# Kernel optimization log

Measured on AMD Instinct MI355X. Metric: run time of the kernel, lower is better.

## Reference

```python
import jax, jax.numpy as jnp
import numpy as np

K = 3
BN_EPS = 1e-3


def setup_inputs() -> dict:
    key = jax.random.key(0)
    ks = jax.random.split(key, 13)
    B, N1, N2 = 8, 1024, 4096
    C1, C2, Cs = 256, 128, 64
    Ctot = C1 + C2 + Cs  # 448
    H = 256
    return {
        "points1": jax.random.normal(ks[0], (B, 3, N1), jnp.float32),
        "points2": jax.random.normal(ks[1], (B, 3, N2), jnp.float32),
        "features1": jax.random.normal(ks[2], (B, C1, N1), jnp.float32),
        "features2": jax.random.normal(ks[3], (B, C2, N2), jnp.float32),
        "skip_features": jax.random.normal(ks[4], (B, Cs, N2), jnp.float32),
        # 1x1 Conv2d weights are equivalent to dense matrices [out, in]
        "W1": jax.random.normal(ks[5], (H, Ctot), jnp.float32) * 0.05,
        "b1": jax.random.normal(ks[6], (H,), jnp.float32) * 0.05,
        "g1": 1.0 + jax.random.normal(ks[7], (H,), jnp.float32) * 0.05,
        "beta1": jax.random.normal(ks[8], (H,), jnp.float32) * 0.05,
        "W2": jax.random.normal(ks[9], (H, H), jnp.float32) * 0.05,
        "b2": jax.random.normal(ks[10], (H,), jnp.float32) * 0.05,
        "g2": 1.0 + jax.random.normal(ks[11], (H,), jnp.float32) * 0.05,
        "beta2": jax.random.normal(ks[12], (H,), jnp.float32) * 0.05,
    }


def _conv_bn_relu(x, W, b, g, beta):
    # x: [B, N, Cin]; 1x1 conv == dense matmul per point
    y = jnp.einsum("bnc,oc->bno", x, W) + b
    # BatchNorm2d in training mode: batch stats over (batch, spatial) per channel
    mu = jnp.mean(y, axis=(0, 1))
    var = jnp.mean(jnp.square(y - mu), axis=(0, 1))  # biased variance
    y = (y - mu) * jax.lax.rsqrt(var + BN_EPS) * g + beta
    return jax.nn.relu(y)


def reference(points1, points2, features1, features2, skip_features,
              W1, b1, g1, beta1, W2, b2, g2, beta2):
    p1 = jnp.swapaxes(points1, 1, 2)  # [B, N1, 3]
    p2 = jnp.swapaxes(points2, 1, 2)  # [B, N2, 3]
    # pairwise Euclidean distances [B, N2, N1]
    d2 = (jnp.sum(p2 * p2, -1, keepdims=True)
          + jnp.sum(p1 * p1, -1)[:, None, :]
          - 2.0 * jnp.einsum("bnd,bmd->bnm", p2, p1))
    dist = jnp.sqrt(jnp.maximum(d2, 0.0))
    # k smallest distances
    neg_top, ind = jax.lax.top_k(-dist, K)  # ind: [B, N2, K]
    dk = -neg_top
    inv = 1.0 / (dk + 1e-10)
    w = inv / jnp.sum(inv, -1, keepdims=True)  # [B, N2, K]
    f1 = jnp.swapaxes(features1, 1, 2)  # [B, N1, C1]
    gathered = jax.vmap(lambda f, i: f[i])(f1, ind)  # [B, N2, K, C1]
    new = jnp.einsum("bnkc,bnk->bnc", gathered, w)  # inverse-distance interp
    x = jnp.concatenate([new,
                         jnp.swapaxes(features2, 1, 2),
                         jnp.swapaxes(skip_features, 1, 2)], axis=-1)
    x = _conv_bn_relu(x, W1, b1, g1, beta1)
    x = _conv_bn_relu(x, W2, b2, g2, beta2)
    return jnp.swapaxes(x, 1, 2)  # [B, Cout, N2]
```

## Files before the change

### kernel.cpp

```cpp
#include <hip/hip_runtime.h>
#include <cstdint>
#include <cstddef>

#define B_    8
#define N1_   1024
#define N2_   4096
#define C1_   256
#define C2_   128
#define CS_   64
#define CT_   448
#define H_    256
#define ROWS_ (B_ * N2_)

typedef __attribute__((ext_vector_type(8))) short bf16x8;
typedef __attribute__((ext_vector_type(4))) float f32x4;
typedef unsigned short ushort_t;
typedef unsigned int   uint_t;

__device__ __forceinline__ ushort_t f2bf(float f) {
    uint_t u = __float_as_uint(f);
    u = (u + 0x7fffu + ((u >> 16) & 1u)) >> 16;
    return (ushort_t)u;
}
__device__ __forceinline__ float bf2f(ushort_t h) {
    return __uint_as_float(((uint_t)h) << 16);
}
__device__ __forceinline__ void glds16(const void* g, void* l) {
    __builtin_amdgcn_global_load_lds(
        (const __attribute__((address_space(1))) void*)g,
        (__attribute__((address_space(3))) void*)l, 16, 0, 0);
}

__global__ __launch_bounds__(256) void fused_pre(
    const float* __restrict__ p1, const float* __restrict__ p2,
    int* __restrict__ ind, float* __restrict__ wout,
    const float* __restrict__ f1, const float* __restrict__ f2,
    const float* __restrict__ fs, const float* __restrict__ W1,
    const float* __restrict__ W2, ushort_t* __restrict__ f1t,
    ushort_t* __restrict__ x, ushort_t* __restrict__ W1b, ushort_t* __restrict__ W2b)
{
#pragma clang fp contract(off)
    __shared__ __align__(16) char smem[32000];
    const int t = threadIdx.x;
    const int bid = blockIdx.x;
    if (bid < 1024) {
        float4*   cand  = (float4*)(smem);
        float*    pvals = (float*)(smem + 16512);
        float*    thr   = (float*)(smem + 19584);
        ushort_t* lists = (ushort_t*)(smem + 19712);
        float*    pdd   = (float*)(smem + 25856);
        int*      pdi   = (int*)(smem + 28928);
        const int b  = bid >> 7;
        const int qb = (bid & 127) * 32;
        const float* pb1 = p1 + (size_t)b * 3 * N1_;
        for (int i = t; i < N1_; i += 256) {
            float X = pb1[i], Y = pb1[N1_ + i], Z = pb1[2 * N1_ + i];
            cand[i] = make_float4(X, Y, Z, (X * X + Y * Y) + Z * Z);
        }
        const int q = t & 31, split = t >> 5;
        const int n = qb + q;
        const float* pb2 = p2 + (size_t)b * 3 * N2_;
        const float ax = pb2[n], ay = pb2[N2_ + n], az = pb2[2 * N2_ + n];
        const float s2a = (ax * ax + ay * ay) + az * az;
        const float m2x = -2.0f * ax, m2y = -2.0f * ay, m2z = -2.0f * az;
        __syncthreads();
        const int ibeg = split * 128, iend = ibeg + 128;
        {
            float a0 = 3e38f, a1 = 3e38f, a2 = 3e38f;
            for (int i = ibeg; i < iend; ++i) {
                float4 c = cand[i];
                float fd = fmaf(c.x, m2x, fmaf(c.y, m2y, fmaf(c.z, m2z, s2a + c.w)));
                float o0 = a0, o1 = a1;
                a0 = fminf(o0, fd);
                a1 = __builtin_amdgcn_fmed3f(fd, o0, o1);
                a2 = __builtin_amdgcn_fmed3f(fd, o1, a2);
            }
            pvals[t * 3 + 0] = a0; pvals[t * 3 + 1] = a1; pvals[t * 3 + 2] = a2;
        }
        __syncthreads();
        if (t < 32) {
            float m0 = 3e38f, m1 = 3e38f, m2v = 3e38f;
#pragma unroll
            for (int g = 0; g < 8; ++g)
#pragma unroll
                for (int r = 0; r < 3; ++r) {
                    float v = pvals[(g * 32 + t) * 3 + r];
                    float o0 = m0, o1 = m1;
                    m0 = fminf(o0, v);
                    m1 = __builtin_amdgcn_fmed3f(v, o0, o1);
                    m2v = __builtin_amdgcn_fmed3f(v, o1, m2v);
                }
            thr[t] = m2v + 2e-3f;
        }
        __syncthreads();
        const float th = thr[q];
        ushort_t* mylist = lists + (q * 8 + split) * 12;
        int cnt = 0;
        for (int i = ibeg; i < iend; ++i) {
            float4 c = cand[i];
            float fd = fmaf(c.x, m2x, fmaf(c.y, m2y, fmaf(c.z, m2z, s2a + c.w)));
            if (fd <= th && cnt < 12) { mylist[cnt] = (ushort_t)i; cnt++; }
        }
        float e0 = 3e38f, e1 = 3e38f, e2 = 3e38f;
        int   j0 = 0, j1 = 0, j2 = 0;
        for (int k = 0; k < cnt; ++k) {
            const int i = mylist[k];
            float4 c = cand[i];
            float dot = (ax * c.x + ay * c.y) + az * c.z;
            float dd  = (s2a + c.w) - 2.0f * dot;
            float d   = sqrtf(fmaxf(dd, 0.0f));
            if (d < e0)      { e2 = e1; j2 = j1; e1 = e0; j1 = j0; e0 = d; j0 = i; }
            else if (d < e1) { e2 = e1; j2 = j1; e1 = d;  j1 = i; }
            else if (d < e2) { e2 = d;  j2 = i; }
        }
        pdd[(split * 32 + q) * 3 + 0] = e0; pdi[(split * 32 + q) * 3 + 0] = j0;
        pdd[(split * 32 + q) * 3 + 1] = e1; pdi[(split * 32 + q) * 3 + 1] = j1;
        pdd[(split * 32 + q) * 3 + 2] = e2; pdi[(split * 32 + q) * 3 + 2] = j2;
        __syncthreads();
        if (t < 32) {
            float f0 = 3e38f, f1v = 3e38f, f2v = 3e38f;
            int   k0 = 0, k1 = 0, k2 = 0;
#pragma unroll
            for (int g = 0; g < 8; ++g)
#pragma unroll
                for (int r = 0; r < 3; ++r) {
                    float d = pdd[(g * 32 + t) * 3 + r];
                    int   i = pdi[(g * 32 + t) * 3 + r];
                    if (d < f0)       { f2v = f1v; k2 = k1; f1v = f0; k1 = k0; f0 = d; k0 = i; }
                    else if (d < f1v) { f2v = f1v; k2 = k1; f1v = d;  k1 = i; }
                    else if (d < f2v) { f2v = d;  k2 = i; }
                }
            float inv0 = 1.0f / (f0 + 1e-10f);
            float inv1 = 1.0f / (f1v + 1e-10f);
            float inv2 = 1.0f / (f2v + 1e-10f);
            float s = (inv0 + inv1) + inv2;
            const size_t row = (size_t)b * N2_ + qb + t;
            wout[row * 3 + 0] = inv0 / s;
            wout[row * 3 + 1] = inv1 / s;
            wout[row * 3 + 2] = inv2 / s;
            ind[row * 3 + 0] = k0;
            ind[row * 3 + 1] = k1;
            ind[row * 3 + 2] = k2;
        }
    } else if (bid < 1536) {
        float (*tile)[65] = (float (*)[65])smem;
        const int bid2 = bid - 1024;
        const int b  = bid2 >> 6;
        const int ct = (bid2 >> 4) & 3;
        const int nt = bid2 & 15;
        const int c0 = ct * 64, n0 = nt * 64;
        const float* src = f1 + ((size_t)b * C1_ + c0) * N1_ + n0;
#pragma unroll
        for (int j = 0; j < 16; ++j) {
            int lin = j * 256 + t;
            int ci = lin >> 6, nj = lin & 63;
            tile[ci][nj] = src[(size_t)ci * N1_ + nj];
        }
        __syncthreads();
        ushort_t* dst = f1t + ((size_t)b * N1_ + n0) * C1_ + c0;
#pragma unroll
        for (int j = 0; j < 8; ++j) {
            int lin = j * 256 + t;
            int ni = lin >> 5, cjp = (lin & 31) * 2;
            uint_t u = (uint_t)f2bf(tile[cjp][ni]) | ((uint_t)f2bf(tile[cjp + 1][ni]) << 16);
            *(uint_t*)&dst[(size_t)ni * C1_ + cjp] = u;
        }
    } else if (bid < 3072) {
        float (*tile)[65] = (float (*)[65])smem;
        const int bid2 = bid - 1536;
        const int b   = bid2 / 192;
        const int rem = bid2 - b * 192;
        const int ct  = rem >> 6;
        const int nt  = rem & 63;
        const float* src;
        int coff;
        if (ct < 2) { src = f2 + ((size_t)b * C2_ + ct * 64) * N2_; coff = C1_ + ct * 64; }
        else        { src = fs + (size_t)b * CS_ * N2_;             coff = C1_ + C2_; }
        const int n0 = nt * 64;
#pragma unroll
        for (int j = 0; j < 16; ++j) {
            int lin = j * 256 + t;
            int ci = lin >> 6, nj = lin & 63;
            tile[ci][nj] = src[(size_t)ci * N2_ + n0 + nj];
        }
        __syncthreads();
#pragma unroll
        for (int j = 0; j < 8; ++j) {
            int lin = j * 256 + t;
            int ni = lin >> 5, cjp = (lin & 31) * 2;
            uint_t u = (uint_t)f2bf(tile[cjp][ni]) | ((uint_t)f2bf(tile[cjp + 1][ni]) << 16);
            *(uint_t*)&x[((size_t)b * N2_ + n0 + ni) * CT_ + coff + cjp] = u;
        }
    } else {
        const int i = (bid - 3072) * 256 + t;
        if (i < H_ * CT_) W1b[i] = f2bf(W1[i]);
        if (i < H_ * H_)  W2b[i] = f2bf(W2[i]);
    }
}

__global__ __launch_bounds__(256) void gather_x(
    const ushort_t* __restrict__ f1t, const int* __restrict__ ind,
    const float* __restrict__ w, ushort_t* __restrict__ x)
{
    const int t = threadIdx.x;
    const int row = blockIdx.x * 8 + (t >> 5);
    const int b = row >> 12;
    const int cg = (t & 31) * 8;
    const int*   ip = ind + (size_t)row * 3;
    const float* wp = w   + (size_t)row * 3;
    const int i0 = ip[0], i1 = ip[1], i2 = ip[2];
    const float w0 = wp[0], w1 = wp[1], w2 = wp[2];
    const ushort_t* base = f1t + (size_t)b * N1_ * C1_;
    uint4 va = *(const uint4*)(base + (size_t)i0 * C1_ + cg);
    uint4 vb = *(const uint4*)(base + (size_t)i1 * C1_ + cg);
    uint4 vc = *(const uint4*)(base + (size_t)i2 * C1_ + cg);
    const uint_t* pa = (const uint_t*)&va;
    const uint_t* pb = (const uint_t*)&vb;
    const uint_t* pc = (const uint_t*)&vc;
    uint_t out[4];
#pragma unroll
    for (int e = 0; e < 4; ++e) {
        float lo = w0 * bf2f((ushort_t)(pa[e] & 0xffff))
                 + w1 * bf2f((ushort_t)(pb[e] & 0xffff))
                 + w2 * bf2f((ushort_t)(pc[e] & 0xffff));
        float hi = w0 * bf2f((ushort_t)(pa[e] >> 16))
                 + w1 * bf2f((ushort_t)(pb[e] >> 16))
                 + w2 * bf2f((ushort_t)(pc[e] >> 16));
        out[e] = (uint_t)f2bf(lo) | ((uint_t)f2bf(hi) << 16);
    }
    *(uint4*)&x[(size_t)row * CT_ + cg] = *(uint4*)out;
}

__global__ __launch_bounds__(256, 4) void gemm1_glds(
    const ushort_t* __restrict__ A, const ushort_t* __restrict__ Bw,
    const float* __restrict__ bias, ushort_t* __restrict__ C,
    float* __restrict__ ssum, float* __restrict__ ssq)
{
    __shared__ __align__(16) ushort_t smem[12288];
    ushort_t* As = smem;
    ushort_t* Bs = smem + 8192;
    ushort_t* Cs = smem;
    const int t = threadIdx.x;
    const int m0 = (blockIdx.x >> 2) * 128;
    const int n0 = (blockIdx.x & 3) * 64;
    const int lane = t & 63;
    const int wv = t >> 6;
    const int wrow = wv & 1, wcol = wv >> 1;
    const int lm = lane & 15, lq = lane >> 4;
    const int lrow8  = lane >> 3;
    const int lchunk = (lane & 7) ^ lrow8;
    const ushort_t* gA = A  + (size_t)(m0 + wv * 32 + lrow8) * CT_ + lchunk * 8;
    const ushort_t* gB = Bw + (size_t)(n0 + wv * 16 + lrow8) * CT_ + lchunk * 8;
    ushort_t* lA = As + wv * 2048;
    ushort_t* lB = Bs + wv * 1024;
    const int aswz = lm & 7;
    f32x4 acc[4][2];
#pragma unroll
    for (int i = 0; i < 4; ++i)
#pragma unroll
        for (int j = 0; j < 2; ++j)
            acc[i][j] = (f32x4){0.f, 0.f, 0.f, 0.f};

    for (int k0 = 0; k0 < CT_; k0 += 64) {
        __syncthreads();
#pragma unroll
        for (int g = 0; g < 4; ++g)
            glds16(gA + k0 + g * 8 * CT_, lA + g * 512);
#pragma unroll
        for (int g = 0; g < 2; ++g)
            glds16(gB + k0 + g * 8 * CT_, lB + g * 512);
        __syncthreads();
#pragma unroll
        for (int h = 0; h < 2; ++h) {
            bf16x8 af[4], bfr[2];
#pragma unroll
            for (int i = 0; i < 4; ++i)
                af[i] = *(const bf16x8*)&As[(wrow * 64 + i * 16 + lm) * 64
                                            + (((h * 4 + lq) ^ aswz)) * 8];
#pragma unroll
            for (int j = 0; j < 2; ++j)
                bfr[j] = *(const bf16x8*)&Bs[(wcol * 32 + j * 16 + lm) * 64
                                             + (((h * 4 + lq) ^ aswz)) * 8];
#pragma unroll
            for (int i = 0; i < 4; ++i)
#pragma unroll
                for (int j = 0; j < 2; ++j)
                    acc[i][j] = __builtin_amdgcn_mfma_f32_16x16x32_bf16(af[i], bfr[j], acc[i][j], 0, 0, 0);
        }
    }
    __syncthreads();
#pragma unroll
    for (int j = 0; j < 2; ++j) {
        const int gn_l = wcol * 32 + j * 16 + lm;
        const int gn   = n0 + gn_l;
        const float bb = bias[gn];
        float ps = 0.0f, pq = 0.0f;
#pragma unroll
        for (int i = 0; i < 4; ++i) {
            const int row_l = wrow * 64 + i * 16 + lq * 4;
            f32x4 v = acc[i][j];
#pragma unroll
            for (int r = 0; r < 4; ++r) {
                float val = v[r] + bb;
                ps += val;
                pq += val * val;
                float vo = __shfl_xor(val, 1);
                uint_t packed = (lm & 1)
                    ? ((uint_t)f2bf(vo)  | ((uint_t)f2bf(val) << 16))
                    : ((uint_t)f2bf(val) | ((uint_t)f2bf(vo)  << 16));
                if ((lm & 1) == 0)
                    *(uint_t*)&Cs[(row_l + r) * 72 + (gn_l & ~1)] = packed;
            }
        }
        ps += __shfl_xor(ps, 16); pq += __shfl_xor(pq, 16);
        ps += __shfl_xor(ps, 32); pq += __shfl_xor(pq, 32);
        if (lane < 16) {
            atomicAdd(&ssum[gn], ps);
            atomicAdd(&ssq[gn], pq);
        }
    }
    __syncthreads();
    const int srow = t >> 3;
    const int scol = (t & 7) * 8;
#pragma unroll
    for (int rep = 0; rep < 4; ++rep) {
        const int row = srow + rep * 32;
        uint4 v = *(const uint4*)&Cs[row * 72 + scol];
        *(uint4*)(C + (size_t)(m0 + row) * H_ + n0 + scol) = v;
    }
}

__global__ __launch_bounds__(256, 4) void gemm2_fused(
    const ushort_t* __restrict__ A, const ushort_t* __restrict__ Bw,
    const float* __restrict__ bias,
    const float* __restrict__ s1, const float* __restrict__ q1,
    const float* __restrict__ g1, const float* __restrict__ be1,
    ushort_t* __restrict__ C, float* __restrict__ ssum, float* __restrict__ ssq)
{
    __shared__ __align__(16) ushort_t smem[15360];
    ushort_t* As0 = smem;
    ushort_t* As1 = smem + 5120;
    ushort_t* Bs  = smem + 10240;
    float*    sc  = (float*)(smem + 14336);
    float*    sh  = (float*)(smem + 14848);
    ushort_t* Cs  = smem;
    const int t = threadIdx.x;
    const int m0 = (blockIdx.x >> 2) * 128;
    const int n0 = (blockIdx.x & 3) * 64;
    const int lane = t & 63;
    const int wv = t >> 6;
    const int wrow = wv & 1, wcol = wv >> 1;
    const int lm = lane & 15, lq = lane >> 4;
    const int lrow8  = lane >> 3;
    const int lchunk = (lane & 7) ^ lrow8;
    const int aswz = lm & 7;
    const int arow = t >> 1, acol = (t & 1) * 32;
    {
        const float invN = 1.0f / (float)ROWS_;
        float mu  = s1[t] * invN;
        float var = q1[t] * invN - mu * mu;
        float s   = rsqrtf(var + 1e-3f) * g1[t];
        sc[t] = s;
        sh[t] = be1[t] - mu * s;
    }
    const ushort_t* gB = Bw + (size_t)(n0 + wv * 16 + lrow8) * H_ + lchunk * 8;
    ushort_t* lB = Bs + wv * 1024;
    const ushort_t* gA = A + (size_t)(m0 + arow) * H_ + acol;
    ushort_t* As_t = (t & 1) ? As1 : As0;
    f32x4 acc[4][2];
#pragma unroll
    for (int i = 0; i < 4; ++i)
#pragma unroll
        for (int j = 0; j < 2; ++j)
            acc[i][j] = (f32x4){0.f, 0.f, 0.f, 0.f};

    for (int k0 = 0; k0 < H_; k0 += 64) {
        uint4 av[4];
#pragma unroll
        for (int g = 0; g < 4; ++g)
            av[g] = *(const uint4*)(gA + k0 + g * 8);
        __syncthreads();
#pragma unroll
        for (int g = 0; g < 2; ++g)
            glds16(gB + k0 + g * 8 * H_, lB + g * 512);
#pragma unroll
        for (int g = 0; g < 4; ++g) {
            const uint_t* wsrc = (const uint_t*)&av[g];
            uint_t o[4];
#pragma unroll
            for (int e = 0; e < 4; ++e) {
                const int cb = k0 + acol + g * 8 + 2 * e;
                float lo = __uint_as_float(wsrc[e] << 16);
                float hi = __uint_as_float(wsrc[e] & 0xffff0000u);
                float r0 = fmaxf(fmaf(lo, sc[cb],     sh[cb]),     0.0f);
                float r1 = fmaxf(fmaf(hi, sc[cb + 1], sh[cb + 1]), 0.0f);
                o[e] = (uint_t)f2bf(r0) | ((uint_t)f2bf(r1) << 16);
            }
            *(uint4*)&As_t[arow * 40 + g * 8] = *(uint4*)o;
        }
        __syncthreads();
#pragma unroll
        for (int h = 0; h < 2; ++h) {
            const ushort_t* Ah = h ? As1 : As0;
            bf16x8 af[4], bfr[2];
#pragma unroll
            for (int i = 0; i < 4; ++i)
                af[i] = *(const bf16x8*)&Ah[(wrow * 64 + i * 16 + lm) * 40 + lq * 8];
#pragma unroll
            for (int j = 0; j < 2; ++j)
                bfr[j] = *(const bf16x8*)&Bs[(wcol * 32 + j * 16 + lm) * 64
                                             + (((h * 4 + lq) ^ aswz)) * 8];
#pragma unroll
            for (int i = 0; i < 4; ++i)
#pragma unroll
                for (int j = 0; j < 2; ++j)
                    acc[i][j] = __builtin_amdgcn_mfma_f32_16x16x32_bf16(af[i], bfr[j], acc[i][j], 0, 0, 0);
        }
    }
    __syncthreads();
#pragma unroll
    for (int j = 0; j < 2; ++j) {
        const int gn_l = wcol * 32 + j * 16 + lm;
        const int gn   = n0 + gn_l;
        const float bb = bias[gn];
        float ps = 0.0f, pq = 0.0f;
#pragma unroll
        for (int i = 0; i < 4; ++i) {
            const int row_l = wrow * 64 + i * 16 + lq * 4;
            f32x4 v = acc[i][j];
#pragma unroll
            for (int r = 0; r < 4; ++r) {
                float val = v[r] + bb;
                ps += val;
                pq += val * val;
                float vo = __shfl_xor(val, 1);
                uint_t packed = (lm & 1)
                    ? ((uint_t)f2bf(vo)  | ((uint_t)f2bf(val) << 16))
                    : ((uint_t)f2bf(val) | ((uint_t)f2bf(vo)  << 16));
                if ((lm & 1) == 0)
                    *(uint_t*)&Cs[(row_l + r) * 72 + (gn_l & ~1)] = packed;
            }
        }
        ps += __shfl_xor(ps, 16); pq += __shfl_xor(pq, 16);
        ps += __shfl_xor(ps, 32); pq += __shfl_xor(pq, 32);
        if (lane < 16) {
            atomicAdd(&ssum[gn], ps);
            atomicAdd(&ssq[gn], pq);
        }
    }
    __syncthreads();
    const int srow = t >> 3;
    const int scol = (t & 7) * 8;
#pragma unroll
    for (int rep = 0; rep < 4; ++rep) {
        const int row = srow + rep * 32;
        uint4 v = *(const uint4*)&Cs[row * 72 + scol];
        *(uint4*)(C + (size_t)(m0 + row) * H_ + n0 + scol) = v;
    }
}

__global__ __launch_bounds__(256) void bn_out_kernel(
    const ushort_t* __restrict__ y, const float* __restrict__ ssum, const float* __restrict__ ssq,
    const float* __restrict__ g, const float* __restrict__ beta, float* __restrict__ out)
{
    __shared__ float tile[64][65];
    __shared__ float sc[64], sh[64];
    const float invN = 1.0f / (float)ROWS_;
    const int bid = blockIdx.x;
    const int b  = bid >> 8;
    const int nt = (bid >> 2) & 63;
    const int ot = bid & 3;
    const int t = threadIdx.x;
    if (t < 64) {
        int c = ot * 64 + t;
        float mu  = ssum[c] * invN;
        float var = ssq[c] * invN - mu * mu;
        float s   = rsqrtf(var + 1e-3f) * g[c];
        sc[t] = s;
        sh[t] = beta[c] - mu * s;
    }
    __syncthreads();
    const int n0 = nt * 64, o0 = ot * 64;
    const ushort_t* yb = y + ((size_t)b * N2_ + n0) * H_ + o0;
#pragma unroll
    for (int j = 0; j < 8; ++j) {
        int lin = j * 256 + t;
        int nl = lin >> 5, cu = (lin & 31) * 2;
        uint_t u = *(const uint_t*)&yb[(size_t)nl * H_ + cu];
        tile[nl][cu]     = fmaxf(bf2f((ushort_t)(u & 0xffff)) * sc[cu]     + sh[cu],     0.0f);
        tile[nl][cu + 1] = fmaxf(bf2f((ushort_t)(u >> 16))    * sc[cu + 1] + sh[cu + 1], 0.0f);
    }
    __syncthreads();
    float* ob = out + ((size_t)b * H_ + o0) * N2_ + n0;
#pragma unroll
    for (int j = 0; j < 16; ++j) {
        int lin = j * 256 + t;
        int ol = lin >> 6, nl = lin & 63;
        ob[(size_t)ol * N2_ + nl] = tile[nl][ol];
    }
}

extern "C" void kernel_launch(void* const* d_in, const int* in_sizes, int n_in,
                              void* d_out, int out_size, void* d_ws, size_t ws_size,
                              hipStream_t stream)
{
    (void)in_sizes; (void)n_in; (void)out_size; (void)ws_size;
    const float* points1   = (const float*)d_in[0];
    const float* points2   = (const float*)d_in[1];
    const float* features1 = (const float*)d_in[2];
    const float* features2 = (const float*)d_in[3];
    const float* skipf     = (const float*)d_in[4];
    const float* W1  = (const float*)d_in[5];
    const float* b1  = (const float*)d_in[6];
    const float* g1  = (const float*)d_in[7];
    const float* be1 = (const float*)d_in[8];
    const float* W2  = (const float*)d_in[9];
    const float* b2  = (const float*)d_in[10];
    const float* g2  = (const float*)d_in[11];
    const float* be2 = (const float*)d_in[12];
    float* out = (float*)d_out;

    char* ws = (char*)d_ws;
    float*    s1  = (float*)(ws + 0);
    float*    q1  = (float*)(ws + 1024);
    float*    s2  = (float*)(ws + 2048);
    float*    q2  = (float*)(ws + 3072);
    int*      ind = (int*)(ws + 4096);
    float*    wgt = (float*)(ws + 397312);
    ushort_t* x   = (ushort_t*)(ws + 790528);
    ushort_t* y1b = (ushort_t*)(ws + 30150656);
    ushort_t* W1b = (ushort_t*)(ws + 63705088);
    ushort_t* W2b = (ushort_t*)(ws + 63934464);
    ushort_t* f1t = (ushort_t*)(ws + 64065536);
    ushort_t* y2b = x;

    hipMemsetAsync(ws, 0, 4096, stream);

    fused_pre<<<dim3(3520), dim3(256), 0, stream>>>(points1, points2, ind, wgt,
                                                    features1, features2, skipf,
                                                    W1, W2, f1t, x, W1b, W2b);
    gather_x<<<dim3(4096), dim3(256), 0, stream>>>(f1t, ind, wgt, x);

    gemm1_glds<<<dim3(ROWS_ / 128 * 4), dim3(256), 0, stream>>>(x, W1b, b1, y1b, s1, q1);
    gemm2_fused<<<dim3(ROWS_ / 128 * 4), dim3(256), 0, stream>>>(y1b, W2b, b2, s1, q1, g1, be1, y2b, s2, q2);
    bn_out_kernel<<<dim3(2048), dim3(256), 0, stream>>>(y2b, s2, q2, g2, be2, out);
}
```

Baseline: 199.0 us.

## Fuse inverse-distance gather into first GEMM A-tile loading

Result: faster. 190.6 us (-4.2%).

```diff
diff --git a/kernel.cpp b/kernel.cpp
--- a/kernel.cpp
+++ b/kernel.cpp
@@ -11,6 +11,7 @@
 #define CT_   448
 #define H_    256
 #define ROWS_ (B_ * N2_)
+#define XW_   192
 
 typedef __attribute__((ext_vector_type(8))) short bf16x8;
 typedef __attribute__((ext_vector_type(4))) float f32x4;
@@ -173,9 +174,9 @@
         const int ct  = rem >> 6;
         const int nt  = rem & 63;
         const float* src;
-        int coff;
-        if (ct < 2) { src = f2 + ((size_t)b * C2_ + ct * 64) * N2_; coff = C1_ + ct * 64; }
-        else        { src = fs + (size_t)b * CS_ * N2_;             coff = C1_ + C2_; }
+        if (ct < 2) src = f2 + ((size_t)b * C2_ + ct * 64) * N2_;
+        else        src = fs + (size_t)b * CS_ * N2_;
+        const int coff = ct * 64;
         const int n0 = nt * 64;
 #pragma unroll
         for (int j = 0; j < 16; ++j) {
@@ -189,7 +190,7 @@
             int lin = j * 256 + t;
             int ni = lin >> 5, cjp = (lin & 31) * 2;
             uint_t u = (uint_t)f2bf(tile[cjp][ni]) | ((uint_t)f2bf(tile[cjp + 1][ni]) << 16);
-            *(uint_t*)&x[((size_t)b * N2_ + n0 + ni) * CT_ + coff + cjp] = u;
+            *(uint_t*)&x[((size_t)b * N2_ + n0 + ni) * XW_ + coff + cjp] = u;
         }
     } else {
         const int i = (bid - 3072) * 256 + t;
@@ -198,43 +199,11 @@
     }
 }
 
-__global__ __launch_bounds__(256) void gather_x(
+__global__ __launch_bounds__(256, 4) void gemm1_fused(
     const ushort_t* __restrict__ f1t, const int* __restrict__ ind,
-    const float* __restrict__ w, ushort_t* __restrict__ x)
-{
-    const int t = threadIdx.x;
-    const int row = blockIdx.x * 8 + (t >> 5);
-    const int b = row >> 12;
-    const int cg = (t & 31) * 8;
-    const int*   ip = ind + (size_t)row * 3;
-    const float* wp = w   + (size_t)row * 3;
-    const int i0 = ip[0], i1 = ip[1], i2 = ip[2];
-    const float w0 = wp[0], w1 = wp[1], w2 = wp[2];
-    const ushort_t* base = f1t + (size_t)b * N1_ * C1_;
-    uint4 va = *(const uint4*)(base + (size_t)i0 * C1_ + cg);
-    uint4 vb = *(const uint4*)(base + (size_t)i1 * C1_ + cg);
-    uint4 vc = *(const uint4*)(base + (size_t)i2 * C1_ + cg);
-    const uint_t* pa = (const uint_t*)&va;
-    const uint_t* pb = (const uint_t*)&vb;
-    const uint_t* pc = (const uint_t*)&vc;
-    uint_t out[4];
-#pragma unroll
-    for (int e = 0; e < 4; ++e) {
-        float lo = w0 * bf2f((ushort_t)(pa[e] & 0xffff))
-                 + w1 * bf2f((ushort_t)(pb[e] & 0xffff))
-                 + w2 * bf2f((ushort_t)(pc[e] & 0xffff));
-        float hi = w0 * bf2f((ushort_t)(pa[e] >> 16))
-                 + w1 * bf2f((ushort_t)(pb[e] >> 16))
-                 + w2 * bf2f((ushort_t)(pc[e] >> 16));
-        out[e] = (uint_t)f2bf(lo) | ((uint_t)f2bf(hi) << 16);
-    }
-    *(uint4*)&x[(size_t)row * CT_ + cg] = *(uint4*)out;
-}
-
-__global__ __launch_bounds__(256, 4) void gemm1_glds(
-    const ushort_t* __restrict__ A, const ushort_t* __restrict__ Bw,
-    const float* __restrict__ bias, ushort_t* __restrict__ C,
-    float* __restrict__ ssum, float* __restrict__ ssq)
+    const float* __restrict__ wgt, const ushort_t* __restrict__ x2,
+    const ushort_t* __restrict__ Bw, const float* __restrict__ bias,
+    ushort_t* __restrict__ C, float* __restrict__ ssum, float* __restrict__ ssq)
 {
     __shared__ __align__(16) ushort_t smem[12288];
     ushort_t* As = smem;
@@ -249,11 +218,24 @@
     const int lm = lane & 15, lq = lane >> 4;
     const int lrow8  = lane >> 3;
     const int lchunk = (lane & 7) ^ lrow8;
-    const ushort_t* gA = A  + (size_t)(m0 + wv * 32 + lrow8) * CT_ + lchunk * 8;
+    const int aswz = lm & 7;
     const ushort_t* gB = Bw + (size_t)(n0 + wv * 16 + lrow8) * CT_ + lchunk * 8;
+    ushort_t* lB = Bs + wv * 1024;
+    const ushort_t* gA = x2 + (size_t)(m0 + wv * 32 + lrow8) * XW_ + lchunk * 8;
     ushort_t* lA = As + wv * 2048;
-    ushort_t* lB = Bs + wv * 1024;
-    const int aswz = lm & 7;
+    const int arow  = t >> 1;
+    const int acolc = (t & 1) * 4;
+    const size_t grow = (size_t)m0 + arow;
+    const int bb_ = (int)(grow >> 12);
+    const int* ip = ind + grow * 3;
+    const float* wp = wgt + grow * 3;
+    const ushort_t* fb = f1t + (size_t)bb_ * N1_ * C1_;
+    const ushort_t* ga0 = fb + (size_t)ip[0] * C1_ + acolc * 8;
+    const ushort_t* ga1 = fb + (size_t)ip[1] * C1_ + acolc * 8;
+    const ushort_t* ga2 = fb + (size_t)ip[2] * C1_ + acolc * 8;
+    const float w0 = wp[0], w1 = wp[1], w2 = wp[2];
+    ushort_t* awr = As + arow * 64;
+    const int arsw = arow & 7;
     f32x4 acc[4][2];
 #pragma unroll
     for (int i = 0; i < 4; ++i)
@@ -263,9 +245,33 @@
 
     for (int k0 = 0; k0 < CT_; k0 += 64) {
         __syncthreads();
-#pragma unroll
-        for (int g = 0; g < 4; ++g)
-            glds16(gA + k0 + g * 8 * CT_, lA + g * 512);
+        if (k0 < 256) {
+#pragma unroll
+            for (int g = 0; g < 4; ++g) {
+                uint4 va = *(const uint4*)(ga0 + k0 + g * 8);
+                uint4 vb = *(const uint4*)(ga1 + k0 + g * 8);
+                uint4 vc = *(const uint4*)(ga2 + k0 + g * 8);
+                const uint_t* pa = (const uint_t*)&va;
+                const uint_t* pb = (const uint_t*)&vb;
+                const uint_t* pc = (const uint_t*)&vc;
+                uint_t o[4];
+#pragma unroll
+                for (int e = 0; e < 4; ++e) {
+                    float lo = w0 * bf2f((ushort_t)(pa[e] & 0xffff))
+                             + w1 * bf2f((ushort_t)(pb[e] & 0xffff))
+                             + w2 * bf2f((ushort_t)(pc[e] & 0xffff));
+                    float hi = w0 * bf2f((ushort_t)(pa[e] >> 16))
+                             + w1 * bf2f((ushort_t)(pb[e] >> 16))
+                             + w2 * bf2f((ushort_t)(pc[e] >> 16));
+                    o[e] = (uint_t)f2bf(lo) | ((uint_t)f2bf(hi) << 16);
+                }
+                *(uint4*)&awr[((acolc + g) ^ arsw) * 8] = *(uint4*)o;
+            }
+        } else {
+#pragma unroll
+            for (int g = 0; g < 4; ++g)
+                glds16(gA + (k0 - 256) + g * 8 * XW_, lA + g * 512);
+        }
 #pragma unroll
         for (int g = 0; g < 2; ++g)
             glds16(gB + k0 + g * 8 * CT_, lB + g * 512);
@@ -539,9 +545,9 @@
     fused_pre<<<dim3(3520), dim3(256), 0, stream>>>(points1, points2, ind, wgt,
                                                     features1, features2, skipf,
                                                     W1, W2, f1t, x, W1b, W2b);
-    gather_x<<<dim3(4096), dim3(256), 0, stream>>>(f1t, ind, wgt, x);
-
-    gemm1_glds<<<dim3(ROWS_ / 128 * 4), dim3(256), 0, stream>>>(x, W1b, b1, y1b, s1, q1);
+
+    gemm1_fused<<<dim3(ROWS_ / 128 * 4), dim3(256), 0, stream>>>(f1t, ind, wgt, x,
+                                                                 W1b, b1, y1b, s1, q1);
     gemm2_fused<<<dim3(ROWS_ / 128 * 4), dim3(256), 0, stream>>>(y1b, W2b, b2, s1, q1, g1, be1, y2b, s2, q2);
     bn_out_kernel<<<dim3(2048), dim3(256), 0, stream>>>(y2b, s2, q2, g2, be2, out);
 }
```
